# Kernel optimization log

Measured on AMD Instinct MI355X. Metric: run time of the kernel, lower is better.

## Reference

```python
import jax, jax.numpy as jnp
import numpy as np

N, M, D = 8192, 8192, 64

def softplus(x):
    # transform_forward in pmf-automl
    return jnp.logaddexp(x, 0.0)

def inv_softplus(y):
    # transform_backward: log(exp(y) - 1), stable form
    return y + jnp.log(-jnp.expm1(-y))

def setup_inputs() -> dict:
    key = jax.random.key(0)
    k1, k2 = jax.random.split(key)
    X = jax.random.normal(k1, (N, D), dtype=jnp.float32)
    X2 = jax.random.normal(k2, (M, D), dtype=jnp.float32)
    # raw (pre-softplus) parameters, matching torch init: softplus(raw)=1
    lengthscale = jnp.full((1, D), inv_softplus(jnp.float32(1.0)), dtype=jnp.float32)
    variance = jnp.full((1,), inv_softplus(jnp.float32(1.0)), dtype=jnp.float32)
    return {"X": X, "X2": X2, "lengthscale": lengthscale, "variance": variance}

def reference(X, X2, lengthscale, variance):
    l = softplus(lengthscale)           # [1, D]
    v = softplus(variance)              # [1]
    Xl = X / l                          # [N, D]
    X2l = X2 / l                        # [M, D]
    xn = jnp.sum(Xl * Xl, axis=1)       # [N]
    yn = jnp.sum(X2l * X2l, axis=1)     # [M]
    cross = Xl @ X2l.T                  # [N, M]
    d2 = jnp.maximum(xn[:, None] + yn[None, :] - 2.0 * cross, 0.0)
    return v[0] * jnp.exp(-0.5 * d2)
```

## Files before the change

kernel.cpp:

```cpp
#include <hip/hip_runtime.h>
#include <math.h>

#define NN 8192
#define MM 8192
#define DD 64
#define BM 128
#define BN 128
#define STR 72

typedef __bf16 bf16x8 __attribute__((ext_vector_type(8)));
typedef __bf16 bf16x4 __attribute__((ext_vector_type(4)));
typedef float f32x4 __attribute__((ext_vector_type(4)));

__device__ __forceinline__ float softplus_f(float x) {
    return fmaxf(x, 0.0f) + log1pf(exp2f(-fabsf(x) * 1.4426950408889634f));
}

__global__ __launch_bounds__(256, 2)
void rbf_mfma_kernel(const float* __restrict__ X, const float* __restrict__ X2,
                     const float* __restrict__ raw_l, const float* __restrict__ raw_v,
                     float* __restrict__ out) {
    __shared__ __bf16 Ah[BM][STR];
    __shared__ __bf16 Al[BM][STR];
    __shared__ __bf16 Bh[BN][STR];
    __shared__ __bf16 Bl[BN][STR];
    __shared__ float ls[DD];
    __shared__ float xn[BM];
    __shared__ float yn[BN];

    const int t  = threadIdx.x;
    const int bn = blockIdx.x;
    const int bm = blockIdx.y;

    if (t < DD) ls[t] = 1.0f / softplus_f(raw_l[t]);
    __syncthreads();

    const int k4 = t & 15;
    const int r0 = t >> 4;
    const float il0 = ls[4 * k4 + 0];
    const float il1 = ls[4 * k4 + 1];
    const float il2 = ls[4 * k4 + 2];
    const float il3 = ls[4 * k4 + 3];

    const float* Xb  = X  + (size_t)(bm * BM) * DD;
    const float* X2b = X2 + (size_t)(bn * BN) * DD;

#pragma unroll
    for (int r = 0; r < 8; ++r) {
        const int row = r0 + 16 * r;
        {
            float4 a = *(const float4*)(Xb + row * DD + 4 * k4);
            a.x *= il0; a.y *= il1; a.z *= il2; a.w *= il3;
            bf16x4 h, l;
            h[0] = (__bf16)a.x; l[0] = (__bf16)(a.x - (float)h[0]);
            h[1] = (__bf16)a.y; l[1] = (__bf16)(a.y - (float)h[1]);
            h[2] = (__bf16)a.z; l[2] = (__bf16)(a.z - (float)h[2]);
            h[3] = (__bf16)a.w; l[3] = (__bf16)(a.w - (float)h[3]);
            *(bf16x4*)&Ah[row][4 * k4] = h;
            *(bf16x4*)&Al[row][4 * k4] = l;
        }
        {
            float4 b = *(const float4*)(X2b + row * DD + 4 * k4);
            b.x *= il0; b.y *= il1; b.z *= il2; b.w *= il3;
            bf16x4 h, l;
            h[0] = (__bf16)b.x; l[0] = (__bf16)(b.x - (float)h[0]);
            h[1] = (__bf16)b.y; l[1] = (__bf16)(b.y - (float)h[1]);
            h[2] = (__bf16)b.z; l[2] = (__bf16)(b.z - (float)h[2]);
            h[3] = (__bf16)b.w; l[3] = (__bf16)(b.w - (float)h[3]);
            *(bf16x4*)&Bh[row][4 * k4] = h;
            *(bf16x4*)&Bl[row][4 * k4] = l;
        }
    }

    {
        const int rowl = t & 127;
        const float* p = (t < 128) ? (Xb + rowl * DD) : (X2b + rowl * DD);
        float s = 0.0f;
#pragma unroll
        for (int j = 0; j < 16; ++j) {
            float4 a = *(const float4*)(p + 4 * j);
            float e;
            e = a.x * ls[4 * j + 0]; s = fmaf(e, e, s);
            e = a.y * ls[4 * j + 1]; s = fmaf(e, e, s);
            e = a.z * ls[4 * j + 2]; s = fmaf(e, e, s);
            e = a.w * ls[4 * j + 3]; s = fmaf(e, e, s);
        }
        if (t < 128) xn[rowl] = s; else yn[rowl] = s;
    }
    __syncthreads();

    const int lane = t & 63;
    const int q    = lane >> 4;
    const int r16  = lane & 15;
    const int w    = t >> 6;
    const int row0 = (w >> 1) * 64;
    const int col0 = (w & 1) * 64;

    f32x4 acc[4][4];
#pragma unroll
    for (int mi = 0; mi < 4; ++mi)
#pragma unroll
        for (int ni = 0; ni < 4; ++ni)
#pragma unroll
            for (int r = 0; r < 4; ++r) acc[mi][ni][r] = 0.0f;

#pragma unroll
    for (int kc = 0; kc < 2; ++kc) {
        const int k0 = kc * 32 + q * 8;
        bf16x8 ah[4], al[4], bh[4], bl[4];
#pragma unroll
        for (int i = 0; i < 4; ++i) {
            ah[i] = *(const bf16x8*)&Ah[row0 + i * 16 + r16][k0];
            al[i] = *(const bf16x8*)&Al[row0 + i * 16 + r16][k0];
            bh[i] = *(const bf16x8*)&Bh[col0 + i * 16 + r16][k0];
            bl[i] = *(const bf16x8*)&Bl[col0 + i * 16 + r16][k0];
        }
#pragma unroll
        for (int mi = 0; mi < 4; ++mi) {
#pragma unroll
            for (int ni = 0; ni < 4; ++ni) {
                acc[mi][ni] = __builtin_amdgcn_mfma_f32_16x16x32_bf16(ah[mi], bh[ni], acc[mi][ni], 0, 0, 0);
                acc[mi][ni] = __builtin_amdgcn_mfma_f32_16x16x32_bf16(ah[mi], bl[ni], acc[mi][ni], 0, 0, 0);
                acc[mi][ni] = __builtin_amdgcn_mfma_f32_16x16x32_bf16(al[mi], bh[ni], acc[mi][ni], 0, 0, 0);
            }
        }
    }

    const float v  = softplus_f(raw_v[0]);
    const float ce = -0.5f * 1.4426950408889634f;

#pragma unroll
    for (int mi = 0; mi < 4; ++mi) {
#pragma unroll
        for (int r = 0; r < 4; ++r) {
            const int lrow = row0 + mi * 16 + q * 4 + r;
            const float xr = xn[lrow];
            float* orow = out + (size_t)(bm * BM + lrow) * MM + bn * BN;
#pragma unroll
            for (int ni = 0; ni < 4; ++ni) {
                const int lcol = col0 + ni * 16 + r16;
                float d2 = fmaxf(xr + yn[lcol] - 2.0f * acc[mi][ni][r], 0.0f);
                orow[lcol] = v * exp2f(ce * d2);
            }
        }
    }
}

extern "C" void kernel_launch(void* const* d_in, const int* in_sizes, int n_in,
                              void* d_out, int out_size, void* d_ws, size_t ws_size,
                              hipStream_t stream) {
    const float* X     = (const float*)d_in[0];
    const float* X2    = (const float*)d_in[1];
    const float* raw_l = (const float*)d_in[2];
    const float* raw_v = (const float*)d_in[3];
    float* out = (float*)d_out;

    dim3 grid(MM / BN, NN / BM);
    dim3 block(256);
    rbf_mfma_kernel<<<grid, block, 0, stream>>>(X, X2, raw_l, raw_v, out);
}
```

Measured before the change: 325.7 us.

## Load MFMA operands directly from global, swap operand roles for float4 output stores

Drops the shared-memory staging of the hi/lo bf16 split tiles. Each wave now loads its fragments straight from global memory and splits them in registers. The lengthscale scaling is folded into a single multiply of X by 1/l^2, which avoids scaling X2 at all. The MFMA operands are swapped so each lane holds four consecutive output columns, letting the epilogue write float4 stores instead of scalar ones. The cost is redundant global loads and conversion work, since each row's fragments are now loaded and split by two waves. The bf16 hi/lo split error also changes because the scaling is applied asymmetrically.

```diff
diff --git a/kernel.cpp b/kernel.cpp
--- a/kernel.cpp
+++ b/kernel.cpp
@@ -1,91 +1,56 @@
 #include <hip/hip_runtime.h>
 #include <math.h>
 
-#define NN 8192
 #define MM 8192
 #define DD 64
-#define BM 128
-#define BN 128
-#define STR 72
 
 typedef __bf16 bf16x8 __attribute__((ext_vector_type(8)));
-typedef __bf16 bf16x4 __attribute__((ext_vector_type(4)));
 typedef float f32x4 __attribute__((ext_vector_type(4)));
 
 __device__ __forceinline__ float softplus_f(float x) {
     return fmaxf(x, 0.0f) + log1pf(exp2f(-fabsf(x) * 1.4426950408889634f));
 }
 
+__device__ __forceinline__ void split8(float4 p0, float4 p1, bf16x8& h, bf16x8& l) {
+    h[0] = (__bf16)p0.x; l[0] = (__bf16)(p0.x - (float)h[0]);
+    h[1] = (__bf16)p0.y; l[1] = (__bf16)(p0.y - (float)h[1]);
+    h[2] = (__bf16)p0.z; l[2] = (__bf16)(p0.z - (float)h[2]);
+    h[3] = (__bf16)p0.w; l[3] = (__bf16)(p0.w - (float)h[3]);
+    h[4] = (__bf16)p1.x; l[4] = (__bf16)(p1.x - (float)h[4]);
+    h[5] = (__bf16)p1.y; l[5] = (__bf16)(p1.y - (float)h[5]);
+    h[6] = (__bf16)p1.z; l[6] = (__bf16)(p1.z - (float)h[6]);
+    h[7] = (__bf16)p1.w; l[7] = (__bf16)(p1.w - (float)h[7]);
+}
+
 __global__ __launch_bounds__(256, 2)
-void rbf_mfma_kernel(const float* __restrict__ X, const float* __restrict__ X2,
-                     const float* __restrict__ raw_l, const float* __restrict__ raw_v,
-                     float* __restrict__ out) {
-    __shared__ __bf16 Ah[BM][STR];
-    __shared__ __bf16 Al[BM][STR];
-    __shared__ __bf16 Bh[BN][STR];
-    __shared__ __bf16 Bl[BN][STR];
-    __shared__ float ls[DD];
-    __shared__ float xn[BM];
-    __shared__ float yn[BN];
+void rbf_mfma2(const float* __restrict__ X, const float* __restrict__ X2,
+               const float* __restrict__ raw_l, const float* __restrict__ raw_v,
+               float* __restrict__ out) {
+    __shared__ float ls2[DD];
+    __shared__ float xn[128];
+    __shared__ float yn[128];
 
     const int t  = threadIdx.x;
     const int bn = blockIdx.x;
     const int bm = blockIdx.y;
 
-    if (t < DD) ls[t] = 1.0f / softplus_f(raw_l[t]);
+    if (t < DD) { float il = 1.0f / softplus_f(raw_l[t]); ls2[t] = il * il; }
     __syncthreads();
 
-    const int k4 = t & 15;
-    const int r0 = t >> 4;
-    const float il0 = ls[4 * k4 + 0];
-    const float il1 = ls[4 * k4 + 1];
-    const float il2 = ls[4 * k4 + 2];
-    const float il3 = ls[4 * k4 + 3];
-
-    const float* Xb  = X  + (size_t)(bm * BM) * DD;
-    const float* X2b = X2 + (size_t)(bn * BN) * DD;
-
-#pragma unroll
-    for (int r = 0; r < 8; ++r) {
-        const int row = r0 + 16 * r;
-        {
-            float4 a = *(const float4*)(Xb + row * DD + 4 * k4);
-            a.x *= il0; a.y *= il1; a.z *= il2; a.w *= il3;
-            bf16x4 h, l;
-            h[0] = (__bf16)a.x; l[0] = (__bf16)(a.x - (float)h[0]);
-            h[1] = (__bf16)a.y; l[1] = (__bf16)(a.y - (float)h[1]);
-            h[2] = (__bf16)a.z; l[2] = (__bf16)(a.z - (float)h[2]);
-            h[3] = (__bf16)a.w; l[3] = (__bf16)(a.w - (float)h[3]);
-            *(bf16x4*)&Ah[row][4 * k4] = h;
-            *(bf16x4*)&Al[row][4 * k4] = l;
-        }
-        {
-            float4 b = *(const float4*)(X2b + row * DD + 4 * k4);
-            b.x *= il0; b.y *= il1; b.z *= il2; b.w *= il3;
-            bf16x4 h, l;
-            h[0] = (__bf16)b.x; l[0] = (__bf16)(b.x - (float)h[0]);
-            h[1] = (__bf16)b.y; l[1] = (__bf16)(b.y - (float)h[1]);
-            h[2] = (__bf16)b.z; l[2] = (__bf16)(b.z - (float)h[2]);
-            h[3] = (__bf16)b.w; l[3] = (__bf16)(b.w - (float)h[3]);
-            *(bf16x4*)&Bh[row][4 * k4] = h;
-            *(bf16x4*)&Bl[row][4 * k4] = l;
-        }
-    }
-
     {
-        const int rowl = t & 127;
-        const float* p = (t < 128) ? (Xb + rowl * DD) : (X2b + rowl * DD);
+        const int r = t & 127;
+        const float* p = (t < 128) ? (X + (size_t)(bm * 128 + r) * DD)
+                                   : (X2 + (size_t)(bn * 128 + r) * DD);
         float s = 0.0f;
 #pragma unroll
         for (int j = 0; j < 16; ++j) {
-            float4 a = *(const float4*)(p + 4 * j);
-            float e;
-            e = a.x * ls[4 * j + 0]; s = fmaf(e, e, s);
-            e = a.y * ls[4 * j + 1]; s = fmaf(e, e, s);
-            e = a.z * ls[4 * j + 2]; s = fmaf(e, e, s);
-            e = a.w * ls[4 * j + 3]; s = fmaf(e, e, s);
+            float4 a = ((const float4*)p)[j];
+            s = fmaf(a.x * a.x, ls2[4 * j + 0], s);
+            s = fmaf(a.y * a.y, ls2[4 * j + 1], s);
+            s = fmaf(a.z * a.z, ls2[4 * j + 2], s);
+            s = fmaf(a.w * a.w, ls2[4 * j + 3], s);
         }
-        if (t < 128) xn[rowl] = s; else yn[rowl] = s;
+        if (t < 128) xn[r] = s; else yn[r] = s;
     }
     __syncthreads();
 
@@ -93,35 +58,48 @@
     const int q    = lane >> 4;
     const int r16  = lane & 15;
     const int w    = t >> 6;
-    const int row0 = (w >> 1) * 64;
-    const int col0 = (w & 1) * 64;
+    const int mw   = (w & 1) * 64;
+    const int nw   = (w >> 1) * 64;
+
+    const float* Xb  = X  + (size_t)(bm * 128 + mw) * DD;
+    const float* X2b = X2 + (size_t)(bn * 128 + nw) * DD;
 
     f32x4 acc[4][4];
 #pragma unroll
-    for (int mi = 0; mi < 4; ++mi)
+    for (int ni = 0; ni < 4; ++ni)
 #pragma unroll
-        for (int ni = 0; ni < 4; ++ni)
+        for (int mi = 0; mi < 4; ++mi)
 #pragma unroll
-            for (int r = 0; r < 4; ++r) acc[mi][ni][r] = 0.0f;
+            for (int r = 0; r < 4; ++r) acc[ni][mi][r] = 0.0f;
 
 #pragma unroll
     for (int kc = 0; kc < 2; ++kc) {
         const int k0 = kc * 32 + q * 8;
-        bf16x8 ah[4], al[4], bh[4], bl[4];
+        float4 s0 = *(const float4*)&ls2[k0];
+        float4 s1 = *(const float4*)&ls2[k0 + 4];
+
+        bf16x8 ah[4], al[4], xh[4], xl[4];
 #pragma unroll
         for (int i = 0; i < 4; ++i) {
-            ah[i] = *(const bf16x8*)&Ah[row0 + i * 16 + r16][k0];
-            al[i] = *(const bf16x8*)&Al[row0 + i * 16 + r16][k0];
-            bh[i] = *(const bf16x8*)&Bh[col0 + i * 16 + r16][k0];
-            bl[i] = *(const bf16x8*)&Bl[col0 + i * 16 + r16][k0];
+            const float* pa = X2b + (i * 16 + r16) * DD + k0;
+            float4 p0 = *(const float4*)pa;
+            float4 p1 = *(const float4*)(pa + 4);
+            split8(p0, p1, ah[i], al[i]);
+
+            const float* pb = Xb + (i * 16 + r16) * DD + k0;
+            float4 q0 = *(const float4*)pb;
+            float4 q1 = *(const float4*)(pb + 4);
+            q0.x *= s0.x; q0.y *= s0.y; q0.z *= s0.z; q0.w *= s0.w;
+            q1.x *= s1.x; q1.y *= s1.y; q1.z *= s1.z; q1.w *= s1.w;
+            split8(q0, q1, xh[i], xl[i]);
         }
 #pragma unroll
-        for (int mi = 0; mi < 4; ++mi) {
+        for (int ni = 0; ni < 4; ++ni) {
 #pragma unroll
-            for (int ni = 0; ni < 4; ++ni) {
-                acc[mi][ni] = __builtin_amdgcn_mfma_f32_16x16x32_bf16(ah[mi], bh[ni], acc[mi][ni], 0, 0, 0);
-                acc[mi][ni] = __builtin_amdgcn_mfma_f32_16x16x32_bf16(ah[mi], bl[ni], acc[mi][ni], 0, 0, 0);
-                acc[mi][ni] = __builtin_amdgcn_mfma_f32_16x16x32_bf16(al[mi], bh[ni], acc[mi][ni], 0, 0, 0);
+            for (int mi = 0; mi < 4; ++mi) {
+                acc[ni][mi] = __builtin_amdgcn_mfma_f32_16x16x32_bf16(ah[ni], xh[mi], acc[ni][mi], 0, 0, 0);
+                acc[ni][mi] = __builtin_amdgcn_mfma_f32_16x16x32_bf16(ah[ni], xl[mi], acc[ni][mi], 0, 0, 0);
+                acc[ni][mi] = __builtin_amdgcn_mfma_f32_16x16x32_bf16(al[ni], xh[mi], acc[ni][mi], 0, 0, 0);
             }
         }
     }
@@ -130,18 +108,21 @@
     const float ce = -0.5f * 1.4426950408889634f;
 
 #pragma unroll
-    for (int mi = 0; mi < 4; ++mi) {
+    for (int ni = 0; ni < 4; ++ni) {
+        float4 yv = *(const float4*)&yn[nw + ni * 16 + q * 4];
+        const int ncol = bn * 128 + nw + ni * 16 + q * 4;
 #pragma unroll
-        for (int r = 0; r < 4; ++r) {
-            const int lrow = row0 + mi * 16 + q * 4 + r;
-            const float xr = xn[lrow];
-            float* orow = out + (size_t)(bm * BM + lrow) * MM + bn * BN;
-#pragma unroll
-            for (int ni = 0; ni < 4; ++ni) {
-                const int lcol = col0 + ni * 16 + r16;
-                float d2 = fmaxf(xr + yn[lcol] - 2.0f * acc[mi][ni][r], 0.0f);
-                orow[lcol] = v * exp2f(ce * d2);
-            }
+        for (int mi = 0; mi < 4; ++mi) {
+            const int ml = mw + mi * 16 + r16;
+            const float xr = xn[ml];
+            f32x4 a = acc[ni][mi];
+            float4 o;
+            float d;
+            d = fminf(ce * (xr + yv.x - 2.0f * a[0]), 0.0f); o.x = v * exp2f(d);
+            d = fminf(ce * (xr + yv.y - 2.0f * a[1]), 0.0f); o.y = v * exp2f(d);
+            d = fminf(ce * (xr + yv.z - 2.0f * a[2]), 0.0f); o.z = v * exp2f(d);
+            d = fminf(ce * (xr + yv.w - 2.0f * a[3]), 0.0f); o.w = v * exp2f(d);
+            *(float4*)(out + (size_t)(bm * 128 + ml) * MM + ncol) = o;
         }
     }
 }
@@ -155,7 +136,7 @@
     const float* raw_v = (const float*)d_in[3];
     float* out = (float*)d_out;
 
-    dim3 grid(MM / BN, NN / BM);
+    dim3 grid(MM / 128, MM / 128);
     dim3 block(256);
-    rbf_mfma_kernel<<<grid, block, 0, stream>>>(X, X2, raw_l, raw_v, out);
+    rbf_mfma2<<<grid, block, 0, stream>>>(X, X2, raw_l, raw_v, out);
 }
```

Result: no change. 331.9 us (+1.9%).
